# Kernel optimization log

Hardware: AMD Instinct MI355X
Metric: run time of the kernel (lower is better)

The kernel has to match this reference:

```python
import jax, jax.numpy as jnp
import numpy as np

BN_EPS = 1e-5

def _conv2d(x, w, b, stride, padding, groups=1):
    out = jax.lax.conv_general_dilated(
        x, w, (stride, stride), padding,
        feature_group_count=groups,
        dimension_numbers=('NCHW', 'OIHW', 'NCHW'))
    return out + b[None, :, None, None]

def _bn(x, g, be, m, v):
    # eval-mode BatchNorm2d
    scale = g / jnp.sqrt(v + BN_EPS)
    return (x - m[None, :, None, None]) * scale[None, :, None, None] + be[None, :, None, None]

def _gelu(x):
    return jax.nn.gelu(x, approximate=False)  # torch nn.GELU default = exact erf

def _forward(x, conv0_w, conv0_b, bn0_g, bn0_b, bn0_m, bn0_v,
             dw_w, dw_b, bn1_g, bn1_b, bn1_m, bn1_v,
             pw_w, pw_b, bn2_g, bn2_b, bn2_m, bn2_v,
             lstm_w, lstm_b, fc_w, fc_b):
    B = x.shape[0]
    nh = conv0_w.shape[0]
    # stem: 4x4 stride-4 conv + BN + GELU -> [B, nh, 8, L]
    y = _gelu(_bn(_conv2d(x, conv0_w, conv0_b, 4, 'VALID'),
                  bn0_g, bn0_b, bn0_m, bn0_v))
    D = dw_w.shape[0]
    for i in range(D):  # MicroBlocks: residual depthwise 3x3 then pointwise 1x1
        r = _gelu(_bn(_conv2d(y, dw_w[i][:, None], dw_b[i], 1, [(1, 1), (1, 1)], groups=nh),
                      bn1_g[i], bn1_b[i], bn1_m[i], bn1_v[i]))
        y = y + r
        y = _gelu(_bn(_conv2d(y, pw_w[i][:, :, None, None], pw_b[i], 1, 'VALID'),
                      bn2_g[i], bn2_b[i], bn2_m[i], bn2_v[i]))
    # ConvLSTM: channel dim nh is the time axis; state is [B, F=8, L]
    L = y.shape[3]
    F = lstm_w.shape[0] // 4
    seq = jnp.transpose(y, (1, 0, 2, 3))  # [nh, B, 8, L]
    h0 = jnp.zeros((B, F, L), y.dtype)

    def step(carry, xt):
        h, c = carry
        comb = jnp.concatenate([xt, h], axis=1)  # [B, 16, L]
        # kernel-size-1 Conv1d == per-position matmul
        A = jnp.einsum('oc,bcl->bol', lstm_w, comb) + lstm_b[None, :, None]
        ai, af, ao, ag = jnp.split(A, 4, axis=1)
        nc = jax.nn.sigmoid(af) * c + jax.nn.sigmoid(ai) * jnp.tanh(ag)
        nhd = jax.nn.sigmoid(ao) * jnp.tanh(nc)
        return (nhd, nc), nhd

    _, ys = jax.lax.scan(step, (h0, h0), seq)  # ys: [nh, B, 8, L]
    feat = jnp.transpose(ys, (1, 0, 2, 3)).reshape(B, nh * F, L)
    # adaptive_avg_pool1d to output size L (== input length) is identity;
    # dropout in eval mode is identity.
    logits = jnp.einsum('bcl,nc->bln', feat, fc_w) + fc_b  # [B, L, nclass]
    return logits

def setup_inputs():
    B, W, NH, D, NCLS, F = 32, 1024, 256, 4, 6625, 8
    key = jax.random.key(0)
    ks = jax.random.split(key, 24)
    n = lambda i, shape, s=0.05: jax.random.normal(ks[i], shape, jnp.float32) * s
    return {
        'x': jax.random.normal(ks[0], (B, 3, 32, W), jnp.float32),
        'conv0_w': n(1, (NH, 3, 4, 4)), 'conv0_b': n(2, (NH,)),
        'bn0_g': 1.0 + n(3, (NH,)), 'bn0_b': n(4, (NH,)),
        'bn0_m': n(5, (NH,)), 'bn0_v': 0.5 + jax.random.uniform(ks[6], (NH,), jnp.float32),
        'dw_w': n(7, (D, NH, 3, 3)), 'dw_b': n(8, (D, NH)),
        'bn1_g': 1.0 + n(9, (D, NH)), 'bn1_b': n(10, (D, NH)),
        'bn1_m': n(11, (D, NH)), 'bn1_v': 0.5 + jax.random.uniform(ks[12], (D, NH), jnp.float32),
        'pw_w': n(13, (D, NH, NH)), 'pw_b': n(14, (D, NH)),
        'bn2_g': 1.0 + n(15, (D, NH)), 'bn2_b': n(16, (D, NH)),
        'bn2_m': n(17, (D, NH)), 'bn2_v': 0.5 + jax.random.uniform(ks[18], (D, NH), jnp.float32),
        'lstm_w': n(19, (4 * F, 2 * F), 0.1), 'lstm_b': n(20, (4 * F,)),
        'fc_w': n(21, (NCLS, NH * F), 0.02), 'fc_b': n(22, (NCLS,)),
    }

def reference(x, conv0_w, conv0_b, bn0_g, bn0_b, bn0_m, bn0_v,
              dw_w, dw_b, bn1_g, bn1_b, bn1_m, bn1_v,
              pw_w, pw_b, bn2_g, bn2_b, bn2_m, bn2_v,
              lstm_w, lstm_b, fc_w, fc_b):
    return _forward(x, conv0_w, conv0_b, bn0_g, bn0_b, bn0_m, bn0_v,
                    dw_w, dw_b, bn1_g, bn1_b, bn1_m, bn1_v,
                    pw_w, pw_b, bn2_g, bn2_b, bn2_m, bn2_v,
                    lstm_w, lstm_b, fc_w, fc_b)
```

## Files before the change

kernel.cpp:

```cpp
#include <hip/hip_runtime.h>
#include <hip/hip_bf16.h>
#include <stdint.h>

#define BNEPS 1e-5f

typedef __bf16 bf16x8 __attribute__((ext_vector_type(8)));
typedef float f32x4 __attribute__((ext_vector_type(4)));
typedef unsigned short ushort8 __attribute__((ext_vector_type(8)));

__device__ __forceinline__ float gelu_f(float x) {
    return 0.5f * x * (1.0f + erff(x * 0.70710678118654752440f));
}
__device__ __forceinline__ float sigmoid_f(float x) {
    return 1.0f / (1.0f + __expf(-x));
}
__device__ __forceinline__ float tanh_f(float x) {
    x = fminf(fmaxf(x, -15.0f), 15.0f);
    const float e = __expf(2.0f * x);
    return (e - 1.0f) / (e + 1.0f);
}
__device__ __forceinline__ float bf2f(unsigned short u) {
    return __uint_as_float(((unsigned)u) << 16);
}
__device__ __forceinline__ void async16(const void* g, void* l) {
    __builtin_amdgcn_global_load_lds(
        (const __attribute__((address_space(1))) void*)g,
        (__attribute__((address_space(3))) void*)l,
        16, 0, 0);
}

__global__ __launch_bounds__(256)
void stem_kernel(const float* __restrict__ x, const float* __restrict__ w,
                 const float* __restrict__ cb,
                 const float* __restrict__ bg, const float* __restrict__ bb,
                 const float* __restrict__ bm, const float* __restrict__ bv,
                 __hip_bfloat16* __restrict__ y0)
{
    __shared__ float sw[64 * 48];
    const int ho = blockIdx.x, b = blockIdx.y, co0 = blockIdx.z * 64;
    const int wo = threadIdx.x;
    for (int i = threadIdx.x; i < 64 * 48; i += 256) sw[i] = w[co0 * 48 + i];
    float p[48];
    #pragma unroll
    for (int c = 0; c < 3; ++c)
        #pragma unroll
        for (int kh = 0; kh < 4; ++kh) {
            const float4 q = *reinterpret_cast<const float4*>(
                &x[((size_t)(b * 3 + c) * 32 + ho * 4 + kh) * 1024 + wo * 4]);
            p[c * 16 + kh * 4 + 0] = q.x;
            p[c * 16 + kh * 4 + 1] = q.y;
            p[c * 16 + kh * 4 + 2] = q.z;
            p[c * 16 + kh * 4 + 3] = q.w;
        }
    __syncthreads();
    for (int c2 = 0; c2 < 64; ++c2) {
        const int co = co0 + c2;
        const float* wp = &sw[c2 * 48];
        float a0 = 0.f, a1 = 0.f, a2 = 0.f, a3 = 0.f;
        #pragma unroll
        for (int i = 0; i < 12; ++i) {
            const float4 wq = *reinterpret_cast<const float4*>(&wp[i * 4]);
            a0 += wq.x * p[i * 4 + 0];
            a1 += wq.y * p[i * 4 + 1];
            a2 += wq.z * p[i * 4 + 2];
            a3 += wq.w * p[i * 4 + 3];
        }
        const float acc = (a0 + a1) + (a2 + a3) + cb[co];
        const float sc = bg[co] / sqrtf(bv[co] + BNEPS);
        const float val = (acc - bm[co]) * sc + bb[co];
        y0[((size_t)(b * 256 + co) * 8 + ho) * 256 + wo] = __float2bfloat16(gelu_f(val));
    }
}

__global__ __launch_bounds__(256)
void dw_kernel(const __hip_bfloat16* __restrict__ y0, const float* __restrict__ dww,
               const float* __restrict__ dwb,
               const float* __restrict__ bg, const float* __restrict__ bb,
               const float* __restrict__ bm, const float* __restrict__ bv,
               __hip_bfloat16* __restrict__ y1)
{
    __shared__ float tile[8][258];
    const int c = blockIdx.x, b = blockIdx.y, t = threadIdx.x;
    const __hip_bfloat16* src = &y0[(size_t)(b * 256 + c) * 2048];
    {
        const ushort8 v = *reinterpret_cast<const ushort8*>(&src[t * 8]);
        const int r = t >> 5, c0 = (t & 31) * 8;
        #pragma unroll
        for (int i = 0; i < 8; ++i) tile[r][1 + c0 + i] = bf2f(v[i]);
    }
    if (t < 8) { tile[t][0] = 0.f; tile[t][257] = 0.f; }
    float w9[9];
    #pragma unroll
    for (int i = 0; i < 9; ++i) w9[i] = dww[c * 9 + i];
    const float bias = dwb[c];
    const float sc = bg[c] / sqrtf(bv[c] + BNEPS);
    const float sb = bb[c] - bm[c] * sc;
    __syncthreads();
    __hip_bfloat16* dst = &y1[(size_t)(b * 256 + c) * 2048];
    #pragma unroll
    for (int r = 0; r < 8; ++r) {
        float acc = bias;
        #pragma unroll
        for (int kh = 0; kh < 3; ++kh) {
            const int rr = r + kh - 1;
            if (rr < 0 || rr > 7) continue;
            acc += w9[kh * 3 + 0] * tile[rr][t] + w9[kh * 3 + 1] * tile[rr][t + 1]
                 + w9[kh * 3 + 2] * tile[rr][t + 2];
        }
        const float val = gelu_f(acc * sc + sb);
        dst[r * 256 + t] = __float2bfloat16(tile[r][t + 1] + val);
    }
}

__global__ __launch_bounds__(256)
void tr_kernel(const __hip_bfloat16* __restrict__ y1, __hip_bfloat16* __restrict__ y1t)
{
    __shared__ __hip_bfloat16 tile[64][65];
    const int hw0 = blockIdx.x * 64, c0 = blockIdx.y * 64, b = blockIdx.z;
    const int tx = threadIdx.x & 63, ty = threadIdx.x >> 6;
    const __hip_bfloat16* src = &y1[((size_t)b * 256 + c0) * 2048 + hw0];
    #pragma unroll
    for (int r = ty; r < 64; r += 4) tile[r][tx] = src[(size_t)r * 2048 + tx];
    __syncthreads();
    __hip_bfloat16* dst = &y1t[((size_t)b * 2048 + hw0) * 256 + c0];
    #pragma unroll
    for (int r = ty; r < 64; r += 4) dst[(size_t)r * 256 + tx] = tile[tx][r];
}

__global__ __launch_bounds__(256)
void gemm_pw_kernel(const __hip_bfloat16* __restrict__ A,
                    const __hip_bfloat16* __restrict__ Bt,
                    __hip_bfloat16* __restrict__ out, int K, int NT,
                    const float* __restrict__ q0, const float* __restrict__ q1,
                    const float* __restrict__ q2, const float* __restrict__ q3,
                    const float* __restrict__ q4)
{
    __shared__ __hip_bfloat16 sA[2][4096];
    __shared__ __hip_bfloat16 sB[2][4096];
    const int tid = threadIdx.x;
    const int wave = tid >> 6, lane = tid & 63;
    const int m0 = blockIdx.y * 128, n0 = blockIdx.x * 128;

    auto stage = [&](int buf, int kt) {
        const int k0 = kt << 5;
        #pragma unroll
        for (int r = 0; r < 2; ++r) {
            const int e = wave * 1024 + r * 512 + lane * 8;
            const int row = e >> 5, ko = e & 31;
            async16(&A[(size_t)(m0 + row) * K + k0 + ko], &sA[buf][wave * 1024 + r * 512]);
            async16(&Bt[(size_t)(n0 + row) * K + k0 + ko], &sB[buf][wave * 1024 + r * 512]);
        }
    };

    f32x4 acc[4][4];
    #pragma unroll
    for (int i = 0; i < 4; ++i)
        #pragma unroll
        for (int j = 0; j < 4; ++j) acc[i][j] = (f32x4){0.f, 0.f, 0.f, 0.f};

    stage(0, 0);
    const int wm = wave >> 1, wn = wave & 1;
    const int lrow = lane & 15, lgrp = lane >> 4;
    int cur = 0;
    for (int kt = 0; kt < NT; ++kt) {
        __syncthreads();
        if (kt + 1 < NT) stage(cur ^ 1, kt + 1);
        bf16x8 av[4], bw[4];
        #pragma unroll
        for (int i = 0; i < 4; ++i) {
            av[i] = *reinterpret_cast<const bf16x8*>(&sA[cur][(wm * 64 + i * 16 + lrow) * 32 + lgrp * 8]);
            bw[i] = *reinterpret_cast<const bf16x8*>(&sB[cur][(wn * 64 + i * 16 + lrow) * 32 + lgrp * 8]);
        }
        #pragma unroll
        for (int mi = 0; mi < 4; ++mi)
            #pragma unroll
            for (int ni = 0; ni < 4; ++ni)
                acc[mi][ni] = __builtin_amdgcn_mfma_f32_16x16x32_bf16(av[mi], bw[ni], acc[mi][ni], 0, 0, 0);
        cur ^= 1;
    }

    #pragma unroll
    for (int mi = 0; mi < 4; ++mi) {
        const int rowb = m0 + wm * 64 + mi * 16 + lgrp * 4;
        #pragma unroll
        for (int ni = 0; ni < 4; ++ni) {
            const int col = n0 + wn * 64 + ni * 16 + lrow;
            #pragma unroll
            for (int r = 0; r < 4; ++r) {
                const float v = acc[mi][ni][r];
                const int co = rowb + r;
                const float sc = q1[co] / sqrtf(q4[co] + BNEPS);
                const float sb = q2[co] - q3[co] * sc;
                const float val = gelu_f((v + q0[co]) * sc + sb);
                const int b_ = col >> 11, hw = col & 2047;
                out[((size_t)b_ * 256 + co) * 2048 + hw] = __float2bfloat16(val);
            }
        }
    }
}

__global__ __launch_bounds__(512, 2)
void gemm_fc_kernel(const __hip_bfloat16* __restrict__ A,
                    const __hip_bfloat16* __restrict__ Bt,
                    const float* __restrict__ fcb,
                    float* __restrict__ out)
{
    constexpr int K = 2048, NT = 64, NTILE = 26;
    __shared__ __hip_bfloat16 smem[49152];
    const int tid = threadIdx.x, wave = tid >> 6, lane = tid & 63;
    const int wm = wave >> 2, wn = wave & 3;
    const int r = lane & 15, g = lane >> 4;
    const int swzk = (g ^ ((r >> 1) & 3)) * 8;

    const int bid = blockIdx.x;
    const int swz = (bid & 7) * 104 + (bid >> 3);
    const int m0 = (swz / NTILE) * 256;
    const int n0 = (swz % NTILE) * 256;

    auto stageA = [&](int buf, int kt) {
        #pragma unroll
        for (int r2 = 0; r2 < 2; ++r2) {
            const int e = wave * 128 + r2 * 64 + lane;
            const int row = e >> 2, slot = e & 3;
            const int kg = slot ^ ((row >> 1) & 3);
            async16(&A[(size_t)(m0 + row) * K + kt * 32 + kg * 8],
                    &smem[buf * 8192 + wave * 1024 + r2 * 512]);
        }
    };
    auto stageB = [&](int buf, int kt) {
        #pragma unroll
        for (int r2 = 0; r2 < 2; ++r2) {
            const int e = wave * 128 + r2 * 64 + lane;
            const int row = e >> 2, slot = e & 3;
            const int kg = slot ^ ((row >> 1) & 3);
            async16(&Bt[(size_t)(n0 + row) * K + kt * 32 + kg * 8],
                    &smem[24576 + buf * 8192 + wave * 1024 + r2 * 512]);
        }
    };

    f32x4 acc[8][4];
    #pragma unroll
    for (int i = 0; i < 8; ++i)
        #pragma unroll
        for (int j = 0; j < 4; ++j) acc[i][j] = (f32x4){0.f, 0.f, 0.f, 0.f};

    stageA(0, 0); stageB(0, 0);
    stageA(1, 1); stageB(1, 1);

    int bc = 0;
    for (int kt = 0; kt < NT; ++kt) {
        if (kt < NT - 1) asm volatile("s_waitcnt vmcnt(4)" ::: "memory");
        else             asm volatile("s_waitcnt vmcnt(0)" ::: "memory");
        asm volatile("s_barrier" ::: "memory");

        const int bn = (bc + 2 >= 3) ? bc - 1 : bc + 2;
        if (kt + 2 < NT) stageA(bn, kt + 2);

        const __hip_bfloat16* pA = &smem[bc * 8192];
        const __hip_bfloat16* pB = &smem[24576 + bc * 8192];
        bf16x8 av[8];
        #pragma unroll
        for (int mi = 0; mi < 8; ++mi)
            av[mi] = *reinterpret_cast<const bf16x8*>(&pA[(wm * 128 + mi * 16 + r) * 32 + swzk]);
        bf16x8 b0 = *reinterpret_cast<const bf16x8*>(&pB[(wn * 64 + 0 * 16 + r) * 32 + swzk]);
        bf16x8 b1 = *reinterpret_cast<const bf16x8*>(&pB[(wn * 64 + 1 * 16 + r) * 32 + swzk]);

        __builtin_amdgcn_s_setprio(1);
        #pragma unroll
        for (int mi = 0; mi < 8; ++mi) {
            acc[mi][0] = __builtin_amdgcn_mfma_f32_16x16x32_bf16(av[mi], b0, acc[mi][0], 0, 0, 0);
            acc[mi][1] = __builtin_amdgcn_mfma_f32_16x16x32_bf16(av[mi], b1, acc[mi][1], 0, 0, 0);
        }
        __builtin_amdgcn_s_setprio(0);

        if (kt + 2 < NT) stageB(bn, kt + 2);
        bf16x8 b2 = *reinterpret_cast<const bf16x8*>(&pB[(wn * 64 + 2 * 16 + r) * 32 + swzk]);
        bf16x8 b3 = *reinterpret_cast<const bf16x8*>(&pB[(wn * 64 + 3 * 16 + r) * 32 + swzk]);

        __builtin_amdgcn_s_setprio(1);
        #pragma unroll
        for (int mi = 0; mi < 8; ++mi) {
            acc[mi][2] = __builtin_amdgcn_mfma_f32_16x16x32_bf16(av[mi], b2, acc[mi][2], 0, 0, 0);
            acc[mi][3] = __builtin_amdgcn_mfma_f32_16x16x32_bf16(av[mi], b3, acc[mi][3], 0, 0, 0);
        }
        __builtin_amdgcn_s_setprio(0);

        bc = (bc == 2) ? 0 : bc + 1;
    }

    #pragma unroll
    for (int mi = 0; mi < 8; ++mi) {
        const int rowb = m0 + wm * 128 + mi * 16 + g * 4;
        #pragma unroll
        for (int ni = 0; ni < 4; ++ni) {
            const int col = n0 + wn * 64 + ni * 16 + r;
            if (col < 6625) {
                const float bb = fcb[col];
                #pragma unroll
                for (int rr = 0; rr < 4; ++rr)
                    out[(size_t)(rowb + rr) * 6625 + col] = acc[mi][ni][rr] + bb;
            }
        }
    }
}

__global__ __launch_bounds__(256)
void lstm_kernel(const __hip_bfloat16* __restrict__ y, const float* __restrict__ lw,
                 const float* __restrict__ lb, __hip_bfloat16* __restrict__ Am)
{
    const int gid = blockIdx.x * 256 + threadIdx.x;
    const int f = gid & 7, pos = gid >> 3;
    const int l = pos & 255, b = pos >> 8;
    float W[4][16], bias[4];
    #pragma unroll
    for (int g = 0; g < 4; ++g) {
        #pragma unroll
        for (int j = 0; j < 16; ++j) W[g][j] = lw[(g * 8 + f) * 16 + j];
        bias[g] = lb[g * 8 + f];
    }
    float h = 0.f, c = 0.f;
    const __hip_bfloat16* xb = y + (size_t)b * 524288 + f * 256 + l;
    __hip_bfloat16* ob = Am + (size_t)pos * 2048 + f;
    float xn = __bfloat162float(xb[0]);
    for (int t = 0; t < 256; ++t) {
        const float xt = xn;
        if (t < 255) xn = __bfloat162float(xb[(size_t)(t + 1) * 2048]);
        float A0 = bias[0], A1 = bias[1], A2 = bias[2], A3 = bias[3];
        #pragma unroll
        for (int j = 0; j < 8; ++j) {
            const float xj = __shfl(xt, j, 8);
            const float hj = __shfl(h, j, 8);
            A0 += W[0][j] * xj + W[0][8 + j] * hj;
            A1 += W[1][j] * xj + W[1][8 + j] * hj;
            A2 += W[2][j] * xj + W[2][8 + j] * hj;
            A3 += W[3][j] * xj + W[3][8 + j] * hj;
        }
        c = sigmoid_f(A1) * c + sigmoid_f(A0) * tanh_f(A3);
        h = sigmoid_f(A2) * tanh_f(c);
        ob[t * 8] = __float2bfloat16(h);
    }
}

__global__ void cvt_pww_kernel(const float* __restrict__ w, __hip_bfloat16* __restrict__ o, int n)
{
    const int i = blockIdx.x * 256 + threadIdx.x;
    if (i < n) o[i] = __float2bfloat16(w[i]);
}
__global__ void cvt_fcw_kernel(const float* __restrict__ w, __hip_bfloat16* __restrict__ o)
{
    const size_t i = (size_t)blockIdx.x * 256 + threadIdx.x;
    const size_t nrow = i >> 11, k = i & 2047;
    o[i] = (nrow < 6625) ? __float2bfloat16(w[nrow * 2048 + k]) : __float2bfloat16(0.0f);
}

extern "C" void kernel_launch(void* const* d_in, const int* in_sizes, int n_in,
                              void* d_out, int out_size, void* d_ws, size_t ws_size,
                              hipStream_t stream)
{
    const float* x       = (const float*)d_in[0];
    const float* conv0_w = (const float*)d_in[1];
    const float* conv0_b = (const float*)d_in[2];
    const float* bn0_g   = (const float*)d_in[3];
    const float* bn0_b   = (const float*)d_in[4];
    const float* bn0_m   = (const float*)d_in[5];
    const float* bn0_v   = (const float*)d_in[6];
    const float* dw_w    = (const float*)d_in[7];
    const float* dw_b    = (const float*)d_in[8];
    const float* bn1_g   = (const float*)d_in[9];
    const float* bn1_b   = (const float*)d_in[10];
    const float* bn1_m   = (const float*)d_in[11];
    const float* bn1_v   = (const float*)d_in[12];
    const float* pw_w    = (const float*)d_in[13];
    const float* pw_b    = (const float*)d_in[14];
    const float* bn2_g   = (const float*)d_in[15];
    const float* bn2_b   = (const float*)d_in[16];
    const float* bn2_m   = (const float*)d_in[17];
    const float* bn2_v   = (const float*)d_in[18];
    const float* lstm_w  = (const float*)d_in[19];
    const float* lstm_b  = (const float*)d_in[20];
    const float* fc_w    = (const float*)d_in[21];
    const float* fc_b    = (const float*)d_in[22];

    char* ws = (char*)d_ws;
    __hip_bfloat16* y0   = (__hip_bfloat16*)(ws);
    __hip_bfloat16* y1   = (__hip_bfloat16*)(ws + 33554432);
    __hip_bfloat16* y1t  = (__hip_bfloat16*)(ws + 67108864);
    __hip_bfloat16* Am   = (__hip_bfloat16*)(ws + 100663296);
    __hip_bfloat16* fcwb = (__hip_bfloat16*)(ws + 134217728);
    __hip_bfloat16* pwwb = (__hip_bfloat16*)(ws + 161480704);

    stem_kernel<<<dim3(8, 32, 4), 256, 0, stream>>>(
        x, conv0_w, conv0_b, bn0_g, bn0_b, bn0_m, bn0_v, y0);
    cvt_pww_kernel<<<1024, 256, 0, stream>>>(pw_w, pwwb, 262144);
    cvt_fcw_kernel<<<53248, 256, 0, stream>>>(fc_w, fcwb);

    for (int i = 0; i < 4; ++i) {
        dw_kernel<<<dim3(256, 32), 256, 0, stream>>>(
            y0, dw_w + i * 2304, dw_b + i * 256,
            bn1_g + i * 256, bn1_b + i * 256, bn1_m + i * 256, bn1_v + i * 256, y1);
        tr_kernel<<<dim3(32, 4, 32), 256, 0, stream>>>(y1, y1t);
        gemm_pw_kernel<<<dim3(512, 2), 256, 0, stream>>>(
            pwwb + i * 65536, y1t, y0, 256, 8,
            pw_b + i * 256, bn2_g + i * 256, bn2_b + i * 256, bn2_m + i * 256, bn2_v + i * 256);
    }

    lstm_kernel<<<256, 256, 0, stream>>>(y0, lstm_w, lstm_b, Am);

    gemm_fc_kernel<<<832, 512, 0, stream>>>(Am, fcwb, fc_b, (float*)d_out);
}
```

Baseline: 688.1 us.

## Fuse depthwise conv with transpose and stage LSTM input/output through LDS

The depthwise 3x3 conv is merged with the NCHW-to-NHWC transpose, so each block tiles 64 channels by 64 width positions with a halo and writes the transposed layout directly. This removes the separate tr_kernel and the y1 round trip through global memory. The LSTM kernel now processes 32 positions per block: it prefetches time chunks of input into shared memory with async copies and buffers hidden outputs so they are written as coalesced 16-byte stores instead of scattered 2-byte writes. In exchange there are more shared-memory accesses and syncs, and the transposed stores from the fused conv are 2-byte per thread.

```diff
diff --git a/kernel.cpp b/kernel.cpp
--- a/kernel.cpp
+++ b/kernel.cpp
@@ -73,58 +73,68 @@
 }
 
 __global__ __launch_bounds__(256)
-void dw_kernel(const __hip_bfloat16* __restrict__ y0, const float* __restrict__ dww,
-               const float* __restrict__ dwb,
-               const float* __restrict__ bg, const float* __restrict__ bb,
-               const float* __restrict__ bm, const float* __restrict__ bv,
-               __hip_bfloat16* __restrict__ y1)
-{
-    __shared__ float tile[8][258];
-    const int c = blockIdx.x, b = blockIdx.y, t = threadIdx.x;
-    const __hip_bfloat16* src = &y0[(size_t)(b * 256 + c) * 2048];
-    {
-        const ushort8 v = *reinterpret_cast<const ushort8*>(&src[t * 8]);
-        const int r = t >> 5, c0 = (t & 31) * 8;
-        #pragma unroll
-        for (int i = 0; i < 8; ++i) tile[r][1 + c0 + i] = bf2f(v[i]);
-    }
-    if (t < 8) { tile[t][0] = 0.f; tile[t][257] = 0.f; }
+void dwt_kernel(const __hip_bfloat16* __restrict__ y0, const float* __restrict__ dww,
+                const float* __restrict__ dwb,
+                const float* __restrict__ bg, const float* __restrict__ bb,
+                const float* __restrict__ bm, const float* __restrict__ bv,
+                __hip_bfloat16* __restrict__ y1t)
+{
+    __shared__ float xt[64][3][69];
+    const int bx = blockIdx.x;
+    const int h0 = bx >> 2, w0 = (bx & 3) * 64;
+    const int C0 = blockIdx.y * 64, b = blockIdx.z;
+    const int tid = threadIdx.x;
+
+    for (int rd = 0; rd < 6; ++rd) {
+        const int idx = rd * 256 + tid;
+        const int c = idx / 24, rem = idx % 24;
+        const int hr = rem >> 3, wc = rem & 7;
+        const int h = h0 - 1 + hr;
+        float v[8];
+        if (h >= 0 && h < 8) {
+            const ushort8 u = *reinterpret_cast<const ushort8*>(
+                &y0[((size_t)((b * 256 + C0 + c) * 8 + h)) * 256 + w0 + wc * 8]);
+            #pragma unroll
+            for (int j = 0; j < 8; ++j) v[j] = bf2f(u[j]);
+        } else {
+            #pragma unroll
+            for (int j = 0; j < 8; ++j) v[j] = 0.f;
+        }
+        #pragma unroll
+        for (int j = 0; j < 8; ++j) xt[c][hr][1 + wc * 8 + j] = v[j];
+    }
+    if (tid < 192) {
+        const int c = tid / 3, hr = tid % 3;
+        const int h = h0 - 1 + hr;
+        float lv = 0.f, rv = 0.f;
+        if (h >= 0 && h < 8) {
+            const size_t rowb = ((size_t)((b * 256 + C0 + c) * 8 + h)) * 256;
+            if (w0 > 0)        lv = __bfloat162float(y0[rowb + w0 - 1]);
+            if (w0 + 64 < 256) rv = __bfloat162float(y0[rowb + w0 + 64]);
+        }
+        xt[c][hr][0] = lv;
+        xt[c][hr][65] = rv;
+    }
+    const int c = tid & 63, wg = tid >> 6;
     float w9[9];
     #pragma unroll
-    for (int i = 0; i < 9; ++i) w9[i] = dww[c * 9 + i];
-    const float bias = dwb[c];
-    const float sc = bg[c] / sqrtf(bv[c] + BNEPS);
-    const float sb = bb[c] - bm[c] * sc;
+    for (int i = 0; i < 9; ++i) w9[i] = dww[(C0 + c) * 9 + i];
+    const float bias = dwb[C0 + c];
+    const float sc = bg[C0 + c] / sqrtf(bv[C0 + c] + BNEPS);
+    const float sb = bb[C0 + c] - bm[C0 + c] * sc;
     __syncthreads();
-    __hip_bfloat16* dst = &y1[(size_t)(b * 256 + c) * 2048];
-    #pragma unroll
-    for (int r = 0; r < 8; ++r) {
+    #pragma unroll
+    for (int wi = 0; wi < 16; ++wi) {
+        const int w = wg * 16 + wi;
         float acc = bias;
         #pragma unroll
-        for (int kh = 0; kh < 3; ++kh) {
-            const int rr = r + kh - 1;
-            if (rr < 0 || rr > 7) continue;
-            acc += w9[kh * 3 + 0] * tile[rr][t] + w9[kh * 3 + 1] * tile[rr][t + 1]
-                 + w9[kh * 3 + 2] * tile[rr][t + 2];
-        }
+        for (int hr = 0; hr < 3; ++hr)
+            acc += w9[hr * 3 + 0] * xt[c][hr][w] + w9[hr * 3 + 1] * xt[c][hr][w + 1]
+                 + w9[hr * 3 + 2] * xt[c][hr][w + 2];
         const float val = gelu_f(acc * sc + sb);
-        dst[r * 256 + t] = __float2bfloat16(tile[r][t + 1] + val);
-    }
-}
-
-__global__ __launch_bounds__(256)
-void tr_kernel(const __hip_bfloat16* __restrict__ y1, __hip_bfloat16* __restrict__ y1t)
-{
-    __shared__ __hip_bfloat16 tile[64][65];
-    const int hw0 = blockIdx.x * 64, c0 = blockIdx.y * 64, b = blockIdx.z;
-    const int tx = threadIdx.x & 63, ty = threadIdx.x >> 6;
-    const __hip_bfloat16* src = &y1[((size_t)b * 256 + c0) * 2048 + hw0];
-    #pragma unroll
-    for (int r = ty; r < 64; r += 4) tile[r][tx] = src[(size_t)r * 2048 + tx];
-    __syncthreads();
-    __hip_bfloat16* dst = &y1t[((size_t)b * 2048 + hw0) * 256 + c0];
-    #pragma unroll
-    for (int r = ty; r < 64; r += 4) dst[(size_t)r * 256 + tx] = tile[tx][r];
+        y1t[((size_t)(b * 2048 + h0 * 256 + w0 + w)) * 256 + C0 + c] =
+            __float2bfloat16(xt[c][1][w + 1] + val);
+    }
 }
 
 __global__ __launch_bounds__(256)
@@ -308,36 +318,66 @@
 void lstm_kernel(const __hip_bfloat16* __restrict__ y, const float* __restrict__ lw,
                  const float* __restrict__ lb, __hip_bfloat16* __restrict__ Am)
 {
-    const int gid = blockIdx.x * 256 + threadIdx.x;
-    const int f = gid & 7, pos = gid >> 3;
-    const int l = pos & 255, b = pos >> 8;
-    float W[4][16], bias[4];
+    __shared__ __hip_bfloat16 xbuf[8192];
+    __shared__ __hip_bfloat16 hbuf[32 * 264];
+    const int tid = threadIdx.x;
+    const int b = blockIdx.x >> 3, l0 = (blockIdx.x & 7) * 32;
+    const int f = tid & 7, lo = tid >> 3;
+    const int wv = tid >> 6;
+
+    float W[4][16], bias4[4];
     #pragma unroll
     for (int g = 0; g < 4; ++g) {
         #pragma unroll
         for (int j = 0; j < 16; ++j) W[g][j] = lw[(g * 8 + f) * 16 + j];
-        bias[g] = lb[g * 8 + f];
-    }
-    float h = 0.f, c = 0.f;
-    const __hip_bfloat16* xb = y + (size_t)b * 524288 + f * 256 + l;
-    __hip_bfloat16* ob = Am + (size_t)pos * 2048 + f;
-    float xn = __bfloat162float(xb[0]);
-    for (int t = 0; t < 256; ++t) {
-        const float xt = xn;
-        if (t < 255) xn = __bfloat162float(xb[(size_t)(t + 1) * 2048]);
-        float A0 = bias[0], A1 = bias[1], A2 = bias[2], A3 = bias[3];
-        #pragma unroll
-        for (int j = 0; j < 8; ++j) {
-            const float xj = __shfl(xt, j, 8);
-            const float hj = __shfl(h, j, 8);
-            A0 += W[0][j] * xj + W[0][8 + j] * hj;
-            A1 += W[1][j] * xj + W[1][8 + j] * hj;
-            A2 += W[2][j] * xj + W[2][8 + j] * hj;
-            A3 += W[3][j] * xj + W[3][8 + j] * hj;
-        }
-        c = sigmoid_f(A1) * c + sigmoid_f(A0) * tanh_f(A3);
-        h = sigmoid_f(A2) * tanh_f(c);
-        ob[t * 8] = __float2bfloat16(h);
+        bias4[g] = lb[g * 8 + f];
+    }
+    const __hip_bfloat16* yb = y + (size_t)b * 524288 + l0;
+
+    auto stage = [&](int tc) {
+        const int t0 = tc * 32;
+        #pragma unroll
+        for (int rd = 0; rd < 4; ++rd) {
+            const int idx = rd * 256 + tid;
+            const int row = idx >> 2, part = idx & 3;
+            const int tt = row >> 3, f2 = row & 7;
+            async16(&yb[(size_t)(t0 + tt) * 2048 + f2 * 256 + part * 8],
+                    &xbuf[(size_t)(rd * 256 + wv * 64) * 8]);
+        }
+    };
+
+    float h = 0.f, cst = 0.f;
+    stage(0);
+    __syncthreads();
+    for (int tc = 0; tc < 8; ++tc) {
+        const int t0 = tc * 32;
+        for (int tt = 0; tt < 32; ++tt) {
+            const float xt = __bfloat162float(xbuf[tt * 256 + f * 32 + lo]);
+            float A0 = bias4[0], A1 = bias4[1], A2 = bias4[2], A3 = bias4[3];
+            #pragma unroll
+            for (int j = 0; j < 8; ++j) {
+                const float xj = __shfl(xt, j, 8);
+                const float hj = __shfl(h, j, 8);
+                A0 += W[0][j] * xj + W[0][8 + j] * hj;
+                A1 += W[1][j] * xj + W[1][8 + j] * hj;
+                A2 += W[2][j] * xj + W[2][8 + j] * hj;
+                A3 += W[3][j] * xj + W[3][8 + j] * hj;
+            }
+            cst = sigmoid_f(A1) * cst + sigmoid_f(A0) * tanh_f(A3);
+            h = sigmoid_f(A2) * tanh_f(cst);
+            hbuf[tt * 264 + lo * 8 + f] = __float2bfloat16(h);
+        }
+        __syncthreads();
+        if (tc + 1 < 8) stage(tc + 1);
+        #pragma unroll
+        for (int rd = 0; rd < 4; ++rd) {
+            const int idx = rd * 256 + tid;
+            const int l = idx >> 5, part = idx & 31;
+            const bf16x8 vv = *reinterpret_cast<const bf16x8*>(&hbuf[part * 264 + l * 8]);
+            *reinterpret_cast<bf16x8*>(
+                &Am[((size_t)(b * 256 + l0 + l)) * 2048 + (t0 + part) * 8]) = vv;
+        }
+        __syncthreads();
     }
 }
 
@@ -383,8 +423,7 @@
 
     char* ws = (char*)d_ws;
     __hip_bfloat16* y0   = (__hip_bfloat16*)(ws);
-    __hip_bfloat16* y1   = (__hip_bfloat16*)(ws + 33554432);
-    __hip_bfloat16* y1t  = (__hip_bfloat16*)(ws + 67108864);
+    __hip_bfloat16* y1t  = (__hip_bfloat16*)(ws + 33554432);
     __hip_bfloat16* Am   = (__hip_bfloat16*)(ws + 100663296);
     __hip_bfloat16* fcwb = (__hip_bfloat16*)(ws + 134217728);
     __hip_bfloat16* pwwb = (__hip_bfloat16*)(ws + 161480704);
@@ -395,10 +434,9 @@
     cvt_fcw_kernel<<<53248, 256, 0, stream>>>(fc_w, fcwb);
 
     for (int i = 0; i < 4; ++i) {
-        dw_kernel<<<dim3(256, 32), 256, 0, stream>>>(
+        dwt_kernel<<<dim3(32, 4, 32), 256, 0, stream>>>(
             y0, dw_w + i * 2304, dw_b + i * 256,
-            bn1_g + i * 256, bn1_b + i * 256, bn1_m + i * 256, bn1_v + i * 256, y1);
-        tr_kernel<<<dim3(32, 4, 32), 256, 0, stream>>>(y1, y1t);
+            bn1_g + i * 256, bn1_b + i * 256, bn1_m + i * 256, bn1_v + i * 256, y1t);
         gemm_pw_kernel<<<dim3(512, 2), 256, 0, stream>>>(
             pwwb + i * 65536, y1t, y0, 256, 8,
             pw_b + i * 256, bn2_g + i * 256, bn2_b + i * 256, bn2_m + i * 256, bn2_v + i * 256);
```

New measurement: 784.7 us. +14.0%, slower.

## Fuse transpose into pointwise GEMM B-tile staging and vectorize fc weight conversion

Applied to the files above, without the earlier changes.

The separate transpose kernel is removed. The pointwise GEMM now reads the NCHW depthwise output directly and transposes it while staging into shared memory, packing pairs of channels into 32-bit stores. This saves a full round trip of a 32 MB intermediate per block, four times in total. The cost is that B staging now goes through registers synchronously instead of async copies, and the shared-memory writes may hit bank conflicts. Separately, the fc weight conversion now handles four elements per thread with float4 loads.

```diff
diff --git a/kernel.cpp b/kernel.cpp
--- a/kernel.cpp
+++ b/kernel.cpp
@@ -113,24 +113,9 @@
 }
 
 __global__ __launch_bounds__(256)
-void tr_kernel(const __hip_bfloat16* __restrict__ y1, __hip_bfloat16* __restrict__ y1t)
-{
-    __shared__ __hip_bfloat16 tile[64][65];
-    const int hw0 = blockIdx.x * 64, c0 = blockIdx.y * 64, b = blockIdx.z;
-    const int tx = threadIdx.x & 63, ty = threadIdx.x >> 6;
-    const __hip_bfloat16* src = &y1[((size_t)b * 256 + c0) * 2048 + hw0];
-    #pragma unroll
-    for (int r = ty; r < 64; r += 4) tile[r][tx] = src[(size_t)r * 2048 + tx];
-    __syncthreads();
-    __hip_bfloat16* dst = &y1t[((size_t)b * 2048 + hw0) * 256 + c0];
-    #pragma unroll
-    for (int r = ty; r < 64; r += 4) dst[(size_t)r * 256 + tx] = tile[tx][r];
-}
-
-__global__ __launch_bounds__(256)
 void gemm_pw_kernel(const __hip_bfloat16* __restrict__ A,
-                    const __hip_bfloat16* __restrict__ Bt,
-                    __hip_bfloat16* __restrict__ out, int K, int NT,
+                    const __hip_bfloat16* __restrict__ y1,
+                    __hip_bfloat16* __restrict__ out,
                     const float* __restrict__ q0, const float* __restrict__ q1,
                     const float* __restrict__ q2, const float* __restrict__ q3,
                     const float* __restrict__ q4)
@@ -140,17 +125,32 @@
     const int tid = threadIdx.x;
     const int wave = tid >> 6, lane = tid & 63;
     const int m0 = blockIdx.y * 128, n0 = blockIdx.x * 128;
-
-    auto stage = [&](int buf, int kt) {
+    const int b = n0 >> 11, hw0 = n0 & 2047;
+    const __hip_bfloat16* ysrc = y1 + (size_t)b * 524288;
+
+    const int ci2 = tid & 15, pos8 = tid >> 4;
+
+    auto stageA = [&](int buf, int kt) {
         const int k0 = kt << 5;
         #pragma unroll
         for (int r = 0; r < 2; ++r) {
             const int e = wave * 1024 + r * 512 + lane * 8;
             const int row = e >> 5, ko = e & 31;
-            async16(&A[(size_t)(m0 + row) * K + k0 + ko], &sA[buf][wave * 1024 + r * 512]);
-            async16(&Bt[(size_t)(n0 + row) * K + k0 + ko], &sB[buf][wave * 1024 + r * 512]);
+            async16(&A[(size_t)(m0 + row) * 256 + k0 + ko], &sA[buf][wave * 1024 + r * 512]);
         }
     };
+    auto stageB = [&](int buf, int kt) {
+        const int ci0 = kt << 5;
+        const ushort8 u0 = *reinterpret_cast<const ushort8*>(
+            &ysrc[(size_t)(ci0 + 2 * ci2) * 2048 + hw0 + pos8 * 8]);
+        const ushort8 u1 = *reinterpret_cast<const ushort8*>(
+            &ysrc[(size_t)(ci0 + 2 * ci2 + 1) * 2048 + hw0 + pos8 * 8]);
+        #pragma unroll
+        for (int j = 0; j < 8; ++j) {
+            const unsigned pk = (unsigned)u0[j] | ((unsigned)u1[j] << 16);
+            *reinterpret_cast<unsigned*>(&sB[buf][(pos8 * 8 + j) * 32 + 2 * ci2]) = pk;
+        }
+    };
 
     f32x4 acc[4][4];
     #pragma unroll
@@ -158,13 +158,13 @@
         #pragma unroll
         for (int j = 0; j < 4; ++j) acc[i][j] = (f32x4){0.f, 0.f, 0.f, 0.f};
 
-    stage(0, 0);
+    stageA(0, 0); stageB(0, 0);
     const int wm = wave >> 1, wn = wave & 1;
     const int lrow = lane & 15, lgrp = lane >> 4;
     int cur = 0;
-    for (int kt = 0; kt < NT; ++kt) {
+    for (int kt = 0; kt < 8; ++kt) {
         __syncthreads();
-        if (kt + 1 < NT) stage(cur ^ 1, kt + 1);
+        if (kt + 1 < 8) { stageA(cur ^ 1, kt + 1); stageB(cur ^ 1, kt + 1); }
         bf16x8 av[4], bw[4];
         #pragma unroll
         for (int i = 0; i < 4; ++i) {
@@ -184,7 +184,7 @@
         const int rowb = m0 + wm * 64 + mi * 16 + lgrp * 4;
         #pragma unroll
         for (int ni = 0; ni < 4; ++ni) {
-            const int col = n0 + wn * 64 + ni * 16 + lrow;
+            const int hw = hw0 + wn * 64 + ni * 16 + lrow;
             #pragma unroll
             for (int r = 0; r < 4; ++r) {
                 const float v = acc[mi][ni][r];
@@ -192,8 +192,7 @@
                 const float sc = q1[co] / sqrtf(q4[co] + BNEPS);
                 const float sb = q2[co] - q3[co] * sc;
                 const float val = gelu_f((v + q0[co]) * sc + sb);
-                const int b_ = col >> 11, hw = col & 2047;
-                out[((size_t)b_ * 256 + co) * 2048 + hw] = __float2bfloat16(val);
+                out[((size_t)(b * 256 + co)) * 2048 + hw] = __float2bfloat16(val);
             }
         }
     }
@@ -348,9 +347,21 @@
 }
 __global__ void cvt_fcw_kernel(const float* __restrict__ w, __hip_bfloat16* __restrict__ o)
 {
-    const size_t i = (size_t)blockIdx.x * 256 + threadIdx.x;
-    const size_t nrow = i >> 11, k = i & 2047;
-    o[i] = (nrow < 6625) ? __float2bfloat16(w[nrow * 2048 + k]) : __float2bfloat16(0.0f);
+    const size_t i4 = (size_t)blockIdx.x * 256 + threadIdx.x;
+    const size_t base = i4 * 4;
+    const size_t nrow = base >> 11, k = base & 2047;
+    if (nrow < 6625) {
+        const float4 q = *reinterpret_cast<const float4*>(&w[nrow * 2048 + k]);
+        o[base + 0] = __float2bfloat16(q.x);
+        o[base + 1] = __float2bfloat16(q.y);
+        o[base + 2] = __float2bfloat16(q.z);
+        o[base + 3] = __float2bfloat16(q.w);
+    } else {
+        o[base + 0] = __float2bfloat16(0.0f);
+        o[base + 1] = __float2bfloat16(0.0f);
+        o[base + 2] = __float2bfloat16(0.0f);
+        o[base + 3] = __float2bfloat16(0.0f);
+    }
 }
 
 extern "C" void kernel_launch(void* const* d_in, const int* in_sizes, int n_in,
@@ -384,7 +395,6 @@
     char* ws = (char*)d_ws;
     __hip_bfloat16* y0   = (__hip_bfloat16*)(ws);
     __hip_bfloat16* y1   = (__hip_bfloat16*)(ws + 33554432);
-    __hip_bfloat16* y1t  = (__hip_bfloat16*)(ws + 67108864);
     __hip_bfloat16* Am   = (__hip_bfloat16*)(ws + 100663296);
     __hip_bfloat16* fcwb = (__hip_bfloat16*)(ws + 134217728);
     __hip_bfloat16* pwwb = (__hip_bfloat16*)(ws + 161480704);
@@ -392,15 +402,14 @@
     stem_kernel<<<dim3(8, 32, 4), 256, 0, stream>>>(
         x, conv0_w, conv0_b, bn0_g, bn0_b, bn0_m, bn0_v, y0);
     cvt_pww_kernel<<<1024, 256, 0, stream>>>(pw_w, pwwb, 262144);
-    cvt_fcw_kernel<<<53248, 256, 0, stream>>>(fc_w, fcwb);
+    cvt_fcw_kernel<<<13312, 256, 0, stream>>>(fc_w, fcwb);
 
     for (int i = 0; i < 4; ++i) {
         dw_kernel<<<dim3(256, 32), 256, 0, stream>>>(
             y0, dw_w + i * 2304, dw_b + i * 256,
             bn1_g + i * 256, bn1_b + i * 256, bn1_m + i * 256, bn1_v + i * 256, y1);
-        tr_kernel<<<dim3(32, 4, 32), 256, 0, stream>>>(y1, y1t);
         gemm_pw_kernel<<<dim3(512, 2), 256, 0, stream>>>(
-            pwwb + i * 65536, y1t, y0, 256, 8,
+            pwwb + i * 65536, y1, y0,
             pw_b + i * 256, bn2_g + i * 256, bn2_b + i * 256, bn2_m + i * 256, bn2_v + i * 256);
     }
 
```

Result: faster. 644.1 us (median of 3 runs) (-6.4%).
